# Optimization experiments

Measured on AMD Instinct MI355X. Metric: run time of the kernel, lower is better.

The kernel has to match this reference:

```python
import jax, jax.numpy as jnp
import numpy as np

B = 4096          # batch size (positions)
K = 32            # max active features per perspective (<=32 pieces)
NF = 22528        # HalfKAv2_hm real feature count
L1, L2, L3 = 1024, 15, 32
COUNT = 9         # num_ls_buckets


def setup_inputs() -> dict:
    key = jax.random.key(0)
    ks = jax.random.split(key, 12)
    us = (jax.random.uniform(ks[0], (B, 1)) < 0.5).astype(jnp.float32)
    them = 1.0 - us
    white_indices = jax.random.randint(ks[1], (B, K), 0, NF, dtype=jnp.int32)
    black_indices = jax.random.randint(ks[2], (B, K), 0, NF, dtype=jnp.int32)
    white_values = jnp.ones((B, K), jnp.float32)
    black_values = jnp.ones((B, K), jnp.float32)
    layer_stack_indices = jax.random.randint(ks[3], (B,), 0, COUNT, dtype=jnp.int32)
    # parameters
    W_ft = jax.random.normal(ks[4], (NF, L1), jnp.float32) * 0.02
    b_ft = jax.random.normal(ks[5], (L1,), jnp.float32) * 0.05
    W1 = jax.random.normal(ks[6], (L1, COUNT * (L2 + 1)), jnp.float32) * (1.0 / np.sqrt(L1))
    b1 = jnp.zeros((COUNT * (L2 + 1),), jnp.float32)
    W2 = jax.random.normal(ks[7], (2 * L2, COUNT * L3), jnp.float32) * (1.0 / np.sqrt(2 * L2))
    b2 = jnp.zeros((COUNT * L3,), jnp.float32)
    W3 = jax.random.normal(ks[8], (L3, COUNT), jnp.float32) * (1.0 / np.sqrt(L3))
    b3 = jnp.zeros((COUNT,), jnp.float32)
    return dict(us=us, them=them, white_indices=white_indices, white_values=white_values,
                black_indices=black_indices, black_values=black_values,
                layer_stack_indices=layer_stack_indices,
                W_ft=W_ft, b_ft=b_ft, W1=W1, b1=b1, W2=W2, b2=b2, W3=W3, b3=b3)


def _select_bucket(x_flat, idx, count, width):
    # x_flat: [B, count*width] -> per-sample bucket slice [B, width]
    x = x_flat.reshape(-1, count, width)
    return jnp.take_along_axis(x, idx[:, None, None], axis=1)[:, 0]


def reference(us, them, white_indices, white_values, black_indices, black_values,
              layer_stack_indices, W_ft, b_ft, W1, b1, W2, b2, W3, b3):
    # --- feature transformer (embedding-bag: gather + weighted sum + bias) ---
    def ft(idx, vals):
        return jnp.einsum('bk,bkl->bl', vals, W_ft[idx]) + b_ft  # [B, L1]
    wp = ft(white_indices, white_values)
    bp = ft(black_indices, black_values)

    # --- perspective mix + clipped quadratic activation ---
    l0 = us * jnp.concatenate([wp, bp], axis=1) + them * jnp.concatenate([bp, wp], axis=1)
    l0 = jnp.clip(l0, 0.0, 1.0)                     # [B, 2*L1]
    h = L1 // 2
    s0, s1, s2, s3 = l0[:, :h], l0[:, h:2*h], l0[:, 2*h:3*h], l0[:, 3*h:]
    l0p = jnp.concatenate([s0 * s1, s2 * s3], axis=1) * (127.0 / 128.0)  # [B, L1]

    # --- bucketed layer stacks ---
    idx = layer_stack_indices
    l1c = _select_bucket(l0p @ W1 + b1, idx, COUNT, L2 + 1)   # [B, L2+1]
    l1x, l1f = l1c[:, :L2], l1c[:, L2:]                        # skip scalar l1f
    l1x = jnp.clip(l1x, 0.0, 1.0)
    l1x = jnp.concatenate([l1x * l1x, l1x], axis=1) * (127.0 / 128.0)  # [B, 2*L2]
    l2c = _select_bucket(l1x @ W2 + b2, idx, COUNT, L3)
    l2x = jnp.clip(l2c, 0.0, 1.0)
    l3c = _select_bucket(l2x @ W3 + b3, idx, COUNT, 1)         # [B, 1]
    return l3c + l1f
```

## Files before the change

### kernel.cpp

```cpp
#include <hip/hip_runtime.h>

#define BDIM 256

constexpr int K      = 32;
constexpr int L1     = 1024;
constexpr int L2C    = 15;
constexpr int L3C    = 32;
constexpr int COUNT  = 9;
constexpr int NF     = 22528;
constexpr int W1COLS = COUNT * (L2C + 1);
constexpr int W2COLS = COUNT * L3C;

__device__ __forceinline__ float clip01(float x) {
    return fminf(fmaxf(x, 0.0f), 1.0f);
}

__device__ __forceinline__ float ub0(unsigned x) { float r; asm("v_cvt_f32_ubyte0 %0, %1" : "=v"(r) : "v"(x)); return r; }
__device__ __forceinline__ float ub1(unsigned x) { float r; asm("v_cvt_f32_ubyte1 %0, %1" : "=v"(r) : "v"(x)); return r; }
__device__ __forceinline__ float ub2(unsigned x) { float r; asm("v_cvt_f32_ubyte2 %0, %1" : "=v"(r) : "v"(x)); return r; }
__device__ __forceinline__ float ub3(unsigned x) { float r; asm("v_cvt_f32_ubyte3 %0, %1" : "=v"(r) : "v"(x)); return r; }

__global__ __launch_bounds__(256) void quant_w_ft(const float* __restrict__ src,
                                                  unsigned char* __restrict__ dst,
                                                  float* __restrict__ scales,
                                                  int nrows) {
    const int wq   = threadIdx.x >> 6;
    const int lane = threadIdx.x & 63;
    const int row  = blockIdx.x * 4 + wq;
    if (row >= nrows) return;

    const float* s = src + (long)row * L1 + lane * 16;
    float4 v[4];
    v[0] = *(const float4*)(s);
    v[1] = *(const float4*)(s + 4);
    v[2] = *(const float4*)(s + 8);
    v[3] = *(const float4*)(s + 12);

    float m = 0.0f;
    #pragma unroll
    for (int i = 0; i < 4; ++i)
        m = fmaxf(m, fmaxf(fmaxf(fabsf(v[i].x), fabsf(v[i].y)),
                           fmaxf(fabsf(v[i].z), fabsf(v[i].w))));
    #pragma unroll
    for (int off = 32; off >= 1; off >>= 1)
        m = fmaxf(m, __shfl_xor(m, off));

    const float mm    = fmaxf(m, 1e-30f);
    const float scale = mm / 127.0f;
    const float inv   = 127.0f / mm;

    uint4 pk;
    unsigned* pw = (unsigned*)&pk;
    #pragma unroll
    for (int i = 0; i < 4; ++i) {
        int q0 = (int)rintf(v[i].x * inv) + 128;
        int q1 = (int)rintf(v[i].y * inv) + 128;
        int q2 = (int)rintf(v[i].z * inv) + 128;
        int q3 = (int)rintf(v[i].w * inv) + 128;
        q0 = max(0, min(255, q0)); q1 = max(0, min(255, q1));
        q2 = max(0, min(255, q2)); q3 = max(0, min(255, q3));
        pw[i] = (unsigned)q0 | ((unsigned)q1 << 8) |
                ((unsigned)q2 << 16) | ((unsigned)q3 << 24);
    }
    *(uint4*)(dst + (long)row * L1 + lane * 16) = pk;
    if (lane == 0) scales[row] = scale;
}

__global__ __launch_bounds__(BDIM) void nnue_fused_q(
    const float* __restrict__ us,
    const float* __restrict__ them,
    const int*   __restrict__ wi,
    const float* __restrict__ wv,
    const int*   __restrict__ bi,
    const float* __restrict__ bvv,
    const int*   __restrict__ lsi,
    const unsigned char* __restrict__ Wq,
    const float* __restrict__ scl,
    const float* __restrict__ b_ft,
    const float* __restrict__ W1,
    const float* __restrict__ b1,
    const float* __restrict__ W2,
    const float* __restrict__ b2,
    const float* __restrict__ W3,
    const float* __restrict__ b3,
    float* __restrict__ out)
{
    const int b = blockIdx.x;
    const int t = threadIdx.x;

    __shared__ int   s_idx[2 * K];
    __shared__ float s_val[2 * K];
    __shared__ float s_wp[L1];
    __shared__ float s_bp[L1];
    __shared__ float s_red[4 * 16];
    __shared__ float s_v[2 * L2C];
    __shared__ float s_p2[L3C];
    __shared__ float s_l1f;

    if (t < K) {
        const int ii = wi[b * K + t];
        s_idx[t] = ii;
        s_val[t] = wv[b * K + t] * scl[ii];
    } else if (t < 2 * K) {
        const int ii = bi[b * K + (t - K)];
        s_idx[t] = ii;
        s_val[t] = bvv[b * K + (t - K)] * scl[ii];
    }
    __syncthreads();

    const int   half = t >> 7;
    const int   tc   = t & 127;
    const int   c8   = tc * 8;
    const int*   idxs = s_idx + half * K;
    const float* vals = s_val + half * K;

    float acc[8];
    {
        const float4 bf0 = *(const float4*)(b_ft + c8);
        const float4 bf1 = *(const float4*)(b_ft + c8 + 4);
        acc[0] = bf0.x; acc[1] = bf0.y; acc[2] = bf0.z; acc[3] = bf0.w;
        acc[4] = bf1.x; acc[5] = bf1.y; acc[6] = bf1.z; acc[7] = bf1.w;
    }

    float sumvs = 0.0f;
    #pragma unroll 8
    for (int k = 0; k < K; ++k) {
        const float vs = vals[k];
        const uint2 q  = *(const uint2*)(Wq + ((long)idxs[k] << 10) + c8);
        sumvs += vs;
        acc[0] = fmaf(vs, ub0(q.x), acc[0]);
        acc[1] = fmaf(vs, ub1(q.x), acc[1]);
        acc[2] = fmaf(vs, ub2(q.x), acc[2]);
        acc[3] = fmaf(vs, ub3(q.x), acc[3]);
        acc[4] = fmaf(vs, ub0(q.y), acc[4]);
        acc[5] = fmaf(vs, ub1(q.y), acc[5]);
        acc[6] = fmaf(vs, ub2(q.y), acc[6]);
        acc[7] = fmaf(vs, ub3(q.y), acc[7]);
    }
    #pragma unroll
    for (int j = 0; j < 8; ++j) acc[j] = fmaf(sumvs, -128.0f, acc[j]);

    {
        float* dst = (half == 0 ? s_wp : s_bp) + c8;
        #pragma unroll
        for (int j = 0; j < 8; ++j) dst[j] = acc[j];
    }
    __syncthreads();

    const float u   = us[b];
    const float th  = them[b];
    const int   idx = lsi[b];
    const float cc  = 127.0f / 128.0f;

    float p[16];
    #pragma unroll
    for (int j = 0; j < 16; ++j) p[j] = 0.0f;

    const float* W1sel = W1 + idx * (L2C + 1);
    const int e0 = t * 4;
    #pragma unroll
    for (int q = 0; q < 4; ++q) {
        const int e = e0 + q;
        float l0p;
        if (e < 512) {
            const float a0 = clip01(u * s_wp[e]       + th * s_bp[e]);
            const float a1 = clip01(u * s_wp[e + 512] + th * s_bp[e + 512]);
            l0p = a0 * a1;
        } else {
            const int   c   = e - 512;
            const float b0  = clip01(u * s_bp[c] + th * s_wp[c]);
            const float b1v = clip01(u * s_bp[e] + th * s_wp[e]);
            l0p = b0 * b1v;
        }
        l0p *= cc;
        const float* wrow = W1sel + e * W1COLS;
        #pragma unroll
        for (int j = 0; j < 16; ++j) p[j] = fmaf(l0p, wrow[j], p[j]);
    }

    const int lane = t & 63;
    const int wid  = t >> 6;
    #pragma unroll
    for (int j = 0; j < 16; ++j) {
        float v = p[j];
        v += __shfl_down(v, 32);
        v += __shfl_down(v, 16);
        v += __shfl_down(v, 8);
        v += __shfl_down(v, 4);
        v += __shfl_down(v, 2);
        v += __shfl_down(v, 1);
        if (lane == 0) s_red[wid * 16 + j] = v;
    }
    __syncthreads();

    if (t < 16) {
        float x1 = s_red[t] + s_red[16 + t] + s_red[32 + t] + s_red[48 + t]
                 + b1[idx * (L2C + 1) + t];
        if (t == 15) {
            s_l1f = x1;
        } else {
            float cx = clip01(x1);
            s_v[t]       = cx * cx * cc;
            s_v[L2C + t] = cx * cc;
        }
    }
    __syncthreads();

    if (t < L3C) {
        float acc2 = b2[idx * L3C + t];
        #pragma unroll
        for (int r = 0; r < 2 * L2C; ++r)
            acc2 = fmaf(s_v[r], W2[r * W2COLS + idx * L3C + t], acc2);
        s_p2[t] = clip01(acc2) * W3[t * COUNT + idx];
    }
    __syncthreads();

    if (t == 0) {
        float s = 0.0f;
        #pragma unroll
        for (int m = 0; m < L3C; ++m) s += s_p2[m];
        out[b] = s + b3[idx] + s_l1f;
    }
}

__global__ __launch_bounds__(BDIM) void nnue_fused_f(
    const float* __restrict__ us,
    const float* __restrict__ them,
    const int*   __restrict__ wi,
    const float* __restrict__ wv,
    const int*   __restrict__ bi,
    const float* __restrict__ bvv,
    const int*   __restrict__ lsi,
    const float* __restrict__ W_ft,
    const float* __restrict__ b_ft,
    const float* __restrict__ W1,
    const float* __restrict__ b1,
    const float* __restrict__ W2,
    const float* __restrict__ b2,
    const float* __restrict__ W3,
    const float* __restrict__ b3,
    float* __restrict__ out)
{
    const int b = blockIdx.x;
    const int t = threadIdx.x;

    __shared__ int   s_idx[2 * K];
    __shared__ float s_val[2 * K];
    __shared__ float s_l0[2 * L1];
    __shared__ float s_red[4 * 16];
    __shared__ float s_v[2 * L2C];
    __shared__ float s_p2[L3C];
    __shared__ float s_l1f;

    if (t < K)          { s_idx[t] = wi[b * K + t];        s_val[t] = wv[b * K + t]; }
    else if (t < 2 * K) { s_idx[t] = bi[b * K + (t - K)];  s_val[t] = bvv[b * K + (t - K)]; }
    __syncthreads();

    const int c4 = t * 4;
    float4 accW = *(const float4*)(b_ft + c4);
    float4 accB = accW;

    #pragma unroll 8
    for (int k = 0; k < K; ++k) {
        const float  vwk = s_val[k];
        const float  vbk = s_val[K + k];
        const float4 rw  = *(const float4*)(W_ft + ((long)s_idx[k]     << 10) + c4);
        const float4 rb  = *(const float4*)(W_ft + ((long)s_idx[K + k] << 10) + c4);
        accW.x = fmaf(vwk, rw.x, accW.x);
        accW.y = fmaf(vwk, rw.y, accW.y);
        accW.z = fmaf(vwk, rw.z, accW.z);
        accW.w = fmaf(vwk, rw.w, accW.w);
        accB.x = fmaf(vbk, rb.x, accB.x);
        accB.y = fmaf(vbk, rb.y, accB.y);
        accB.z = fmaf(vbk, rb.z, accB.z);
        accB.w = fmaf(vbk, rb.w, accB.w);
    }

    const float u  = us[b];
    const float th = them[b];
    float4 A, Bv;
    A.x  = clip01(u * accW.x + th * accB.x);
    A.y  = clip01(u * accW.y + th * accB.y);
    A.z  = clip01(u * accW.z + th * accB.z);
    A.w  = clip01(u * accW.w + th * accB.w);
    Bv.x = clip01(u * accB.x + th * accW.x);
    Bv.y = clip01(u * accB.y + th * accW.y);
    Bv.z = clip01(u * accB.z + th * accW.z);
    Bv.w = clip01(u * accB.w + th * accW.w);
    *(float4*)(s_l0 + c4)      = A;
    *(float4*)(s_l0 + L1 + c4) = Bv;
    __syncthreads();

    const int   idx = lsi[b];
    const float cc  = 127.0f / 128.0f;

    float p[16];
    #pragma unroll
    for (int j = 0; j < 16; ++j) p[j] = 0.0f;

    const float* W1sel = W1 + idx * (L2C + 1);
    #pragma unroll
    for (int q = 0; q < 4; ++q) {
        const int e = c4 + q;
        float l0p;
        if (e < 512) l0p = s_l0[e] * s_l0[e + 512];
        else         l0p = s_l0[e + 512] * s_l0[e + 1024];
        l0p *= cc;
        const float* wrow = W1sel + e * W1COLS;
        #pragma unroll
        for (int j = 0; j < 16; ++j) p[j] = fmaf(l0p, wrow[j], p[j]);
    }

    const int lane = t & 63;
    const int wid  = t >> 6;
    #pragma unroll
    for (int j = 0; j < 16; ++j) {
        float v = p[j];
        v += __shfl_down(v, 32);
        v += __shfl_down(v, 16);
        v += __shfl_down(v, 8);
        v += __shfl_down(v, 4);
        v += __shfl_down(v, 2);
        v += __shfl_down(v, 1);
        if (lane == 0) s_red[wid * 16 + j] = v;
    }
    __syncthreads();

    if (t < 16) {
        float x1 = s_red[t] + s_red[16 + t] + s_red[32 + t] + s_red[48 + t]
                 + b1[idx * (L2C + 1) + t];
        if (t == 15) {
            s_l1f = x1;
        } else {
            float cx = clip01(x1);
            s_v[t]       = cx * cx * cc;
            s_v[L2C + t] = cx * cc;
        }
    }
    __syncthreads();

    if (t < L3C) {
        float acc = b2[idx * L3C + t];
        #pragma unroll
        for (int r = 0; r < 2 * L2C; ++r)
            acc = fmaf(s_v[r], W2[r * W2COLS + idx * L3C + t], acc);
        s_p2[t] = clip01(acc) * W3[t * COUNT + idx];
    }
    __syncthreads();

    if (t == 0) {
        float s = 0.0f;
        #pragma unroll
        for (int m = 0; m < L3C; ++m) s += s_p2[m];
        out[b] = s + b3[idx] + s_l1f;
    }
}

extern "C" void kernel_launch(void* const* d_in, const int* in_sizes, int n_in,
                              void* d_out, int out_size, void* d_ws, size_t ws_size,
                              hipStream_t stream) {
    const float* us   = (const float*)d_in[0];
    const float* them = (const float*)d_in[1];
    const int*   wi   = (const int*)  d_in[2];
    const float* wv   = (const float*)d_in[3];
    const int*   bi   = (const int*)  d_in[4];
    const float* bv   = (const float*)d_in[5];
    const int*   lsi  = (const int*)  d_in[6];
    const float* W_ft = (const float*)d_in[7];
    const float* b_ft = (const float*)d_in[8];
    const float* W1   = (const float*)d_in[9];
    const float* b1   = (const float*)d_in[10];
    const float* W2   = (const float*)d_in[11];
    const float* b2   = (const float*)d_in[12];
    const float* W3   = (const float*)d_in[13];
    const float* b3   = (const float*)d_in[14];
    float*       out  = (float*)d_out;

    const int Bn = in_sizes[0];
    const size_t qTableBytes = (size_t)NF * L1;
    const size_t needed      = qTableBytes + (size_t)NF * sizeof(float);

    if (ws_size >= needed) {
        unsigned char* Wq  = (unsigned char*)d_ws;
        float*         scl = (float*)((char*)d_ws + qTableBytes);
        quant_w_ft<<<(NF + 3) / 4, 256, 0, stream>>>(W_ft, Wq, scl, NF);
        nnue_fused_q<<<Bn, BDIM, 0, stream>>>(us, them, wi, wv, bi, bv, lsi,
                                              Wq, scl, b_ft, W1, b1, W2, b2, W3, b3, out);
    } else {
        nnue_fused_f<<<Bn, BDIM, 0, stream>>>(us, them, wi, wv, bi, bv, lsi,
                                              W_ft, b_ft, W1, b1, W2, b2, W3, b3, out);
    }
}
```

Before: 231.6 us.

## Process two batch rows per block in quantized fused NNUE kernel

The quantized fused kernel now handles two positions per block. The two embedding-bag gathers are interleaved in one loop to expose more memory-level parallelism, and the dense layer stack then runs sequentially for each row. Byte extraction switches from inline-asm cvt_ubyte to plain shift/mask casts, leaving instruction selection to the compiler. This halves the grid and block-launch overhead, but doubles shared memory and accumulator registers and serialises the small-layer tail within each block.

```diff
diff --git a/kernel.cpp b/kernel.cpp
--- a/kernel.cpp
+++ b/kernel.cpp
@@ -14,11 +14,6 @@
 __device__ __forceinline__ float clip01(float x) {
     return fminf(fmaxf(x, 0.0f), 1.0f);
 }
-
-__device__ __forceinline__ float ub0(unsigned x) { float r; asm("v_cvt_f32_ubyte0 %0, %1" : "=v"(r) : "v"(x)); return r; }
-__device__ __forceinline__ float ub1(unsigned x) { float r; asm("v_cvt_f32_ubyte1 %0, %1" : "=v"(r) : "v"(x)); return r; }
-__device__ __forceinline__ float ub2(unsigned x) { float r; asm("v_cvt_f32_ubyte2 %0, %1" : "=v"(r) : "v"(x)); return r; }
-__device__ __forceinline__ float ub3(unsigned x) { float r; asm("v_cvt_f32_ubyte3 %0, %1" : "=v"(r) : "v"(x)); return r; }
 
 __global__ __launch_bounds__(256) void quant_w_ft(const float* __restrict__ src,
                                                   unsigned char* __restrict__ dst,
@@ -66,7 +61,7 @@
     if (lane == 0) scales[row] = scale;
 }
 
-__global__ __launch_bounds__(BDIM) void nnue_fused_q(
+__global__ __launch_bounds__(BDIM) void nnue_fused_q2(
     const float* __restrict__ us,
     const float* __restrict__ them,
     const int*   __restrict__ wi,
@@ -83,143 +78,173 @@
     const float* __restrict__ b2,
     const float* __restrict__ W3,
     const float* __restrict__ b3,
-    float* __restrict__ out)
+    float* __restrict__ out,
+    int Bn)
 {
-    const int b = blockIdx.x;
-    const int t = threadIdx.x;
-
-    __shared__ int   s_idx[2 * K];
-    __shared__ float s_val[2 * K];
-    __shared__ float s_wp[L1];
-    __shared__ float s_bp[L1];
+    const int t  = threadIdx.x;
+    const int r0 = blockIdx.x * 2;
+    const int r1 = min(r0 + 1, Bn - 1);
+
+    __shared__ int   s_idx[2][2][K];
+    __shared__ float s_val[2][2][K];
+    __shared__ float s_wp[2][L1];
+    __shared__ float s_bp[2][L1];
     __shared__ float s_red[4 * 16];
     __shared__ float s_v[2 * L2C];
     __shared__ float s_p2[L3C];
     __shared__ float s_l1f;
 
-    if (t < K) {
-        const int ii = wi[b * K + t];
-        s_idx[t] = ii;
-        s_val[t] = wv[b * K + t] * scl[ii];
-    } else if (t < 2 * K) {
-        const int ii = bi[b * K + (t - K)];
-        s_idx[t] = ii;
-        s_val[t] = bvv[b * K + (t - K)] * scl[ii];
+    if (t < 128) {
+        const int g     = t >> 5;
+        const int kk    = t & 31;
+        const int row   = g >> 1;
+        const int persp = g & 1;
+        const int brow  = row == 0 ? r0 : r1;
+        int ii; float vv;
+        if (persp == 0) { ii = wi[brow * K + kk]; vv = wv[brow * K + kk]; }
+        else            { ii = bi[brow * K + kk]; vv = bvv[brow * K + kk]; }
+        s_idx[row][persp][kk] = ii;
+        s_val[row][persp][kk] = vv * scl[ii];
     }
     __syncthreads();
 
     const int   half = t >> 7;
     const int   tc   = t & 127;
     const int   c8   = tc * 8;
-    const int*   idxs = s_idx + half * K;
-    const float* vals = s_val + half * K;
-
-    float acc[8];
+    const int*   i0 = s_idx[0][half];
+    const int*   i1 = s_idx[1][half];
+    const float* v0 = s_val[0][half];
+    const float* v1 = s_val[1][half];
+
+    float acc0[8], acc1[8];
     {
         const float4 bf0 = *(const float4*)(b_ft + c8);
         const float4 bf1 = *(const float4*)(b_ft + c8 + 4);
-        acc[0] = bf0.x; acc[1] = bf0.y; acc[2] = bf0.z; acc[3] = bf0.w;
-        acc[4] = bf1.x; acc[5] = bf1.y; acc[6] = bf1.z; acc[7] = bf1.w;
-    }
-
-    float sumvs = 0.0f;
+        acc0[0] = bf0.x; acc0[1] = bf0.y; acc0[2] = bf0.z; acc0[3] = bf0.w;
+        acc0[4] = bf1.x; acc0[5] = bf1.y; acc0[6] = bf1.z; acc0[7] = bf1.w;
+        #pragma unroll
+        for (int j = 0; j < 8; ++j) acc1[j] = acc0[j];
+    }
+
+    float sum0 = 0.0f, sum1 = 0.0f;
     #pragma unroll 8
     for (int k = 0; k < K; ++k) {
-        const float vs = vals[k];
-        const uint2 q  = *(const uint2*)(Wq + ((long)idxs[k] << 10) + c8);
-        sumvs += vs;
-        acc[0] = fmaf(vs, ub0(q.x), acc[0]);
-        acc[1] = fmaf(vs, ub1(q.x), acc[1]);
-        acc[2] = fmaf(vs, ub2(q.x), acc[2]);
-        acc[3] = fmaf(vs, ub3(q.x), acc[3]);
-        acc[4] = fmaf(vs, ub0(q.y), acc[4]);
-        acc[5] = fmaf(vs, ub1(q.y), acc[5]);
-        acc[6] = fmaf(vs, ub2(q.y), acc[6]);
-        acc[7] = fmaf(vs, ub3(q.y), acc[7]);
-    }
-    #pragma unroll
-    for (int j = 0; j < 8; ++j) acc[j] = fmaf(sumvs, -128.0f, acc[j]);
+        const float vs0 = v0[k];
+        const float vs1 = v1[k];
+        const uint2 qa  = *(const uint2*)(Wq + ((long)i0[k] << 10) + c8);
+        const uint2 qb  = *(const uint2*)(Wq + ((long)i1[k] << 10) + c8);
+        sum0 += vs0; sum1 += vs1;
+        acc0[0] = fmaf(vs0, (float)( qa.x        & 0xffu), acc0[0]);
+        acc0[1] = fmaf(vs0, (float)((qa.x >>  8) & 0xffu), acc0[1]);
+        acc0[2] = fmaf(vs0, (float)((qa.x >> 16) & 0xffu), acc0[2]);
+        acc0[3] = fmaf(vs0, (float)( qa.x >> 24        ), acc0[3]);
+        acc0[4] = fmaf(vs0, (float)( qa.y        & 0xffu), acc0[4]);
+        acc0[5] = fmaf(vs0, (float)((qa.y >>  8) & 0xffu), acc0[5]);
+        acc0[6] = fmaf(vs0, (float)((qa.y >> 16) & 0xffu), acc0[6]);
+        acc0[7] = fmaf(vs0, (float)( qa.y >> 24        ), acc0[7]);
+        acc1[0] = fmaf(vs1, (float)( qb.x        & 0xffu), acc1[0]);
+        acc1[1] = fmaf(vs1, (float)((qb.x >>  8) & 0xffu), acc1[1]);
+        acc1[2] = fmaf(vs1, (float)((qb.x >> 16) & 0xffu), acc1[2]);
+        acc1[3] = fmaf(vs1, (float)( qb.x >> 24        ), acc1[3]);
+        acc1[4] = fmaf(vs1, (float)( qb.y        & 0xffu), acc1[4]);
+        acc1[5] = fmaf(vs1, (float)((qb.y >>  8) & 0xffu), acc1[5]);
+        acc1[6] = fmaf(vs1, (float)((qb.y >> 16) & 0xffu), acc1[6]);
+        acc1[7] = fmaf(vs1, (float)( qb.y >> 24        ), acc1[7]);
+    }
+    #pragma unroll
+    for (int j = 0; j < 8; ++j) {
+        acc0[j] = fmaf(sum0, -128.0f, acc0[j]);
+        acc1[j] = fmaf(sum1, -128.0f, acc1[j]);
+    }
 
     {
-        float* dst = (half == 0 ? s_wp : s_bp) + c8;
-        #pragma unroll
-        for (int j = 0; j < 8; ++j) dst[j] = acc[j];
-    }
-    __syncthreads();
-
-    const float u   = us[b];
-    const float th  = them[b];
-    const int   idx = lsi[b];
-    const float cc  = 127.0f / 128.0f;
-
-    float p[16];
-    #pragma unroll
-    for (int j = 0; j < 16; ++j) p[j] = 0.0f;
-
-    const float* W1sel = W1 + idx * (L2C + 1);
-    const int e0 = t * 4;
-    #pragma unroll
-    for (int q = 0; q < 4; ++q) {
-        const int e = e0 + q;
-        float l0p;
-        if (e < 512) {
-            const float a0 = clip01(u * s_wp[e]       + th * s_bp[e]);
-            const float a1 = clip01(u * s_wp[e + 512] + th * s_bp[e + 512]);
-            l0p = a0 * a1;
-        } else {
-            const int   c   = e - 512;
-            const float b0  = clip01(u * s_bp[c] + th * s_wp[c]);
-            const float b1v = clip01(u * s_bp[e] + th * s_wp[e]);
-            l0p = b0 * b1v;
-        }
-        l0p *= cc;
-        const float* wrow = W1sel + e * W1COLS;
-        #pragma unroll
-        for (int j = 0; j < 16; ++j) p[j] = fmaf(l0p, wrow[j], p[j]);
-    }
-
-    const int lane = t & 63;
-    const int wid  = t >> 6;
-    #pragma unroll
-    for (int j = 0; j < 16; ++j) {
-        float v = p[j];
-        v += __shfl_down(v, 32);
-        v += __shfl_down(v, 16);
-        v += __shfl_down(v, 8);
-        v += __shfl_down(v, 4);
-        v += __shfl_down(v, 2);
-        v += __shfl_down(v, 1);
-        if (lane == 0) s_red[wid * 16 + j] = v;
-    }
-    __syncthreads();
-
-    if (t < 16) {
-        float x1 = s_red[t] + s_red[16 + t] + s_red[32 + t] + s_red[48 + t]
-                 + b1[idx * (L2C + 1) + t];
-        if (t == 15) {
-            s_l1f = x1;
-        } else {
-            float cx = clip01(x1);
-            s_v[t]       = cx * cx * cc;
-            s_v[L2C + t] = cx * cc;
-        }
-    }
-    __syncthreads();
-
-    if (t < L3C) {
-        float acc2 = b2[idx * L3C + t];
-        #pragma unroll
-        for (int r = 0; r < 2 * L2C; ++r)
-            acc2 = fmaf(s_v[r], W2[r * W2COLS + idx * L3C + t], acc2);
-        s_p2[t] = clip01(acc2) * W3[t * COUNT + idx];
-    }
-    __syncthreads();
-
-    if (t == 0) {
-        float s = 0.0f;
-        #pragma unroll
-        for (int m = 0; m < L3C; ++m) s += s_p2[m];
-        out[b] = s + b3[idx] + s_l1f;
+        float* d0 = (half == 0 ? s_wp[0] : s_bp[0]) + c8;
+        float* d1 = (half == 0 ? s_wp[1] : s_bp[1]) + c8;
+        #pragma unroll
+        for (int j = 0; j < 8; ++j) { d0[j] = acc0[j]; d1[j] = acc1[j]; }
+    }
+    __syncthreads();
+
+    const float cc   = 127.0f / 128.0f;
+    const int   lane = t & 63;
+    const int   wid  = t >> 6;
+
+    for (int r = 0; r < 2; ++r) {
+        const int   brow = r == 0 ? r0 : r1;
+        const float u    = us[brow];
+        const float th   = them[brow];
+        const int   idx  = lsi[brow];
+        const float* swp = s_wp[r];
+        const float* sbp = s_bp[r];
+
+        float p[16];
+        #pragma unroll
+        for (int j = 0; j < 16; ++j) p[j] = 0.0f;
+
+        const float* W1sel = W1 + idx * (L2C + 1);
+        const int e0 = t * 4;
+        #pragma unroll
+        for (int q = 0; q < 4; ++q) {
+            const int e = e0 + q;
+            float l0p;
+            if (e < 512) {
+                const float a0 = clip01(u * swp[e]       + th * sbp[e]);
+                const float a1 = clip01(u * swp[e + 512] + th * sbp[e + 512]);
+                l0p = a0 * a1;
+            } else {
+                const int   c   = e - 512;
+                const float b0  = clip01(u * sbp[c] + th * swp[c]);
+                const float b1v = clip01(u * sbp[e] + th * swp[e]);
+                l0p = b0 * b1v;
+            }
+            l0p *= cc;
+            const float* wrow = W1sel + e * W1COLS;
+            #pragma unroll
+            for (int j = 0; j < 16; ++j) p[j] = fmaf(l0p, wrow[j], p[j]);
+        }
+
+        #pragma unroll
+        for (int j = 0; j < 16; ++j) {
+            float v = p[j];
+            v += __shfl_down(v, 32);
+            v += __shfl_down(v, 16);
+            v += __shfl_down(v, 8);
+            v += __shfl_down(v, 4);
+            v += __shfl_down(v, 2);
+            v += __shfl_down(v, 1);
+            if (lane == 0) s_red[wid * 16 + j] = v;
+        }
+        __syncthreads();
+
+        if (t < 16) {
+            float x1 = s_red[t] + s_red[16 + t] + s_red[32 + t] + s_red[48 + t]
+                     + b1[idx * (L2C + 1) + t];
+            if (t == 15) {
+                s_l1f = x1;
+            } else {
+                float cx = clip01(x1);
+                s_v[t]       = cx * cx * cc;
+                s_v[L2C + t] = cx * cc;
+            }
+        }
+        __syncthreads();
+
+        if (t < L3C) {
+            float acc2 = b2[idx * L3C + t];
+            #pragma unroll
+            for (int rr = 0; rr < 2 * L2C; ++rr)
+                acc2 = fmaf(s_v[rr], W2[rr * W2COLS + idx * L3C + t], acc2);
+            s_p2[t] = clip01(acc2) * W3[t * COUNT + idx];
+        }
+        __syncthreads();
+
+        if (t == 0 && (r == 0 || r1 != r0)) {
+            float s = 0.0f;
+            #pragma unroll
+            for (int m = 0; m < L3C; ++m) s += s_p2[m];
+            out[brow] = s + b3[idx] + s_l1f;
+        }
+        if (r == 0) __syncthreads();
     }
 }
 
@@ -384,8 +409,9 @@
         unsigned char* Wq  = (unsigned char*)d_ws;
         float*         scl = (float*)((char*)d_ws + qTableBytes);
         quant_w_ft<<<(NF + 3) / 4, 256, 0, stream>>>(W_ft, Wq, scl, NF);
-        nnue_fused_q<<<Bn, BDIM, 0, stream>>>(us, them, wi, wv, bi, bv, lsi,
-                                              Wq, scl, b_ft, W1, b1, W2, b2, W3, b3, out);
+        nnue_fused_q2<<<(Bn + 1) / 2, BDIM, 0, stream>>>(us, them, wi, wv, bi, bv, lsi,
+                                                         Wq, scl, b_ft, W1, b1, W2, b2,
+                                                         W3, b3, out, Bn);
     } else {
         nnue_fused_f<<<Bn, BDIM, 0, stream>>>(us, them, wi, wv, bi, bv, lsi,
                                               W_ft, b_ft, W1, b1, W2, b2, W3, b3, out);
```

Measured after the change: 238.5 us. 3.0% more time.
